# Kernel optimization log

Measured on AMD Instinct MI355X. Metric: run time of the kernel, lower is better.

The kernel has to match this reference:

```python
import jax, jax.numpy as jnp
import numpy as np

D = 1024
H = 16
DK = D // H  # 64
CHUNK = 64
EPS = 1e-5


def setup_inputs() -> dict:
    key = jax.random.key(0)
    k1, k2, k3 = jax.random.split(key, 3)
    x = jax.random.normal(k1, (4, 4096, D), dtype=jnp.float32)
    W_qkv = jax.random.normal(k2, (D, 3 * D), dtype=jnp.float32) * 0.02
    W_o = jax.random.normal(k3, (D, D), dtype=jnp.float32) * 0.02
    return {"x": x, "W_qkv": W_qkv, "W_o": W_o}


def _layernorm_noaffine(k):
    mu = jnp.mean(k, axis=-1, keepdims=True)
    var = jnp.mean((k - mu) ** 2, axis=-1, keepdims=True)  # biased var, torch LayerNorm
    return (k - mu) / jnp.sqrt(var + EPS)


def _linear_attn(x, W_qkv, W_o):
    B, L, Dm = x.shape
    qkv = (x @ W_qkv).reshape(B, L, 3, H, DK)
    q, k, v = qkv[:, :, 0], qkv[:, :, 1], qkv[:, :, 2]
    k = _layernorm_noaffine(k)

    nC = L // CHUNK
    # [nC, B, C, H, DK] for scan over chunks
    to_chunks = lambda t: t.reshape(B, nC, CHUNK, H, DK).transpose(1, 0, 2, 3, 4)
    qc, kc, vc = to_chunks(q), to_chunks(k), to_chunks(v)

    causal = jnp.tril(jnp.ones((CHUNK, CHUNK), dtype=bool))  # s <= t inclusive

    def step(S, chunk):
        q_c, k_c, v_c = chunk  # each [B, C, H, DK]
        # inter-chunk: y_t += S_prev @ q_t
        inter = jnp.einsum('bhde,bthe->bthd', S, q_c)
        # intra-chunk: y_t += sum_{s<=t} (k_s . q_t) v_s
        scores = jnp.einsum('bthd,bshd->bhts', q_c, k_c)
        scores = jnp.where(causal, scores, 0.0)
        intra = jnp.einsum('bhts,bshd->bthd', scores, v_c)
        # state update: S += sum_t v_t k_t^T
        S = S + jnp.einsum('bthd,bthe->bhde', v_c, k_c)
        return S, inter + intra

    S0 = jnp.zeros((B, H, DK, DK), dtype=x.dtype)
    _, ys = jax.lax.scan(step, S0, (qc, kc, vc))  # ys: [nC, B, C, H, DK]
    y = ys.transpose(1, 0, 2, 3, 4).reshape(B, L, Dm)
    return y @ W_o


def reference(x, W_qkv, W_o):
    return _linear_attn(x, W_qkv, W_o)
```

## Files before the change

kernel.cpp:

```cpp
#include <hip/hip_runtime.h>

#define EPS 1e-5f

typedef __attribute__((ext_vector_type(8))) short s16x8;
typedef __attribute__((ext_vector_type(4))) float f4;

__device__ __forceinline__ short f2bf(float f) {
  union { float f; unsigned u; } x; x.f = f;
  unsigned r = x.u + 0x7fffu + ((x.u >> 16) & 1u);
  return (short)(r >> 16);
}
__device__ __forceinline__ float bf2f(short s) {
  union { unsigned u; float f; } x; x.u = ((unsigned)(unsigned short)s) << 16;
  return x.f;
}
__device__ __forceinline__ void gll16(const short* g, short* l) {
  __builtin_amdgcn_global_load_lds((const __attribute__((address_space(1))) void*)g,
                                   (__attribute__((address_space(3))) void*)l, 16, 0, 0);
}

#define BAR() asm volatile("s_barrier" ::: "memory")
#define LGKM0() do { asm volatile("s_waitcnt lgkmcnt(0)" ::: "memory"); \
                     __builtin_amdgcn_sched_barrier(0); } while (0)

__global__ __launch_bounds__(256) void prep(
    const float* __restrict__ x, const float* __restrict__ Wqkv,
    const float* __restrict__ Wo,
    short* __restrict__ xb, short* __restrict__ WqkvT, short* __restrict__ WoT)
{
  __shared__ float tile[32][33];
  const int bid = blockIdx.x;
  if (bid < 8192) {
    const size_t i = ((size_t)bid * 256 + threadIdx.x) * 8;
    const float4* p = reinterpret_cast<const float4*>(x + i);
    float4 a = p[0], b = p[1];
    union { uint4 v; short s[8]; } o;
    o.s[0] = f2bf(a.x); o.s[1] = f2bf(a.y); o.s[2] = f2bf(a.z); o.s[3] = f2bf(a.w);
    o.s[4] = f2bf(b.x); o.s[5] = f2bf(b.y); o.s[6] = f2bf(b.z); o.s[7] = f2bf(b.w);
    *reinterpret_cast<uint4*>(xb + i) = o.v;
    return;
  }
  const float* W; short* WT; int K, N, t;
  if (bid < 11264) { W = Wqkv; WT = WqkvT; K = 1024; N = 3072; t = bid - 8192;  }
  else             { W = Wo;   WT = WoT;   K = 1024; N = 1024; t = bid - 11264; }
  const int nblk = N >> 5;
  const int n0 = (t % nblk) * 32, k0 = (t / nblk) * 32;
  const int tx = threadIdx.x & 31, ty = threadIdx.x >> 5;
  #pragma unroll
  for (int i = 0; i < 4; i++) {
    int r = ty + i * 8;
    tile[r][tx] = W[(size_t)(k0 + r) * N + n0 + tx];
  }
  __syncthreads();
  #pragma unroll
  for (int i = 0; i < 4; i++) {
    int r = ty + i * 8;
    WT[(size_t)(n0 + r) * K + k0 + tx] = f2bf(tile[tx][r]);
  }
}

__device__ __forceinline__ void stage_slice(const short* __restrict__ G, short* dstbase,
                                            int row0, int kcol, int rowgrp, int panel, int lane) {
  short* dst = dstbase + panel * 8192 + rowgrp * 512;
  const short* src = G + (size_t)(row0 + rowgrp * 16 + (lane >> 2)) * 1024
                       + kcol + panel * 32 + (((lane & 3) << 3) ^ ((lane >> 5) << 4));
  gll16(src, dst);
}

template<bool STAGE>
__device__ __forceinline__ void ktile8p(
    const short* ldsAc, const short* ldsBc, short* ldsAn, short* ldsBn,
    const short* __restrict__ A, const short* __restrict__ BT,
    int m0, int n0, int knext,
    int w, int lane, int wm, int wn, int quad, int l16,
    f4 (&acc)[8][4])
{
  s16x8 bfr[4][2];
  const int co = (quad << 3) ^ ((l16 >> 3) << 4);
  #pragma unroll
  for (int p = 0; p < 4; ++p) {
    s16x8 a00, a01, a10, a11;
    {
      const int r0 = (wm * 128 + p * 32 + l16) * 32;
      a00 = *reinterpret_cast<const s16x8*>(&ldsAc[r0 + co]);
      a01 = *reinterpret_cast<const s16x8*>(&ldsAc[8192 + r0 + co]);
      a10 = *reinterpret_cast<const s16x8*>(&ldsAc[r0 + 512 + co]);
      a11 = *reinterpret_cast<const s16x8*>(&ldsAc[8192 + r0 + 512 + co]);
    }
    if (p == 0) {
      #pragma unroll
      for (int nf = 0; nf < 4; ++nf) {
        const int rb = (wn * 64 + nf * 16 + l16) * 32;
        bfr[nf][0] = *reinterpret_cast<const s16x8*>(&ldsBc[rb + co]);
        bfr[nf][1] = *reinterpret_cast<const s16x8*>(&ldsBc[8192 + rb + co]);
      }
    }
    if (STAGE) {
      if (p == 0)      { stage_slice(BT, ldsBn, n0, knext, w,     0, lane); stage_slice(BT, ldsBn, n0, knext, w,     1, lane); }
      else if (p == 1) { stage_slice(BT, ldsBn, n0, knext, 8 + w, 0, lane); stage_slice(BT, ldsBn, n0, knext, 8 + w, 1, lane); }
      else if (p == 2) { const int rg = (w & 3) + ((w >> 2) << 3);
                         stage_slice(A, ldsAn, m0, knext, rg, 0, lane); stage_slice(A, ldsAn, m0, knext, rg, 1, lane); }
      else             { const int rg = 4 + (w & 3) + ((w >> 2) << 3);
                         stage_slice(A, ldsAn, m0, knext, rg, 0, lane); stage_slice(A, ldsAn, m0, knext, rg, 1, lane); }
    }
    BAR();
    LGKM0();
    __builtin_amdgcn_s_setprio(1);
    #pragma unroll
    for (int nf = 0; nf < 4; ++nf) {
      acc[2*p  ][nf] = __builtin_amdgcn_mfma_f32_16x16x32_bf16(a00, bfr[nf][0], acc[2*p  ][nf], 0, 0, 0);
      acc[2*p  ][nf] = __builtin_amdgcn_mfma_f32_16x16x32_bf16(a01, bfr[nf][1], acc[2*p  ][nf], 0, 0, 0);
      acc[2*p+1][nf] = __builtin_amdgcn_mfma_f32_16x16x32_bf16(a10, bfr[nf][0], acc[2*p+1][nf], 0, 0, 0);
      acc[2*p+1][nf] = __builtin_amdgcn_mfma_f32_16x16x32_bf16(a11, bfr[nf][1], acc[2*p+1][nf], 0, 0, 0);
    }
    __builtin_amdgcn_s_setprio(0);
    if (p == 1) {
      if (STAGE) asm volatile("s_waitcnt vmcnt(4)" ::: "memory");
      else       asm volatile("s_waitcnt vmcnt(0)" ::: "memory");
    }
    if (p == 3 && STAGE) asm volatile("s_waitcnt vmcnt(2)" ::: "memory");
    BAR();
  }
}

#define GEMM8P_PROLOGUE()                                                            \
  stage_slice(BT, Bb0, n0, 0, w,     0, lane); stage_slice(BT, Bb0, n0, 0, w,     1, lane); \
  stage_slice(BT, Bb0, n0, 0, 8 + w, 0, lane); stage_slice(BT, Bb0, n0, 0, 8 + w, 1, lane); \
  { const int rg = (w & 3) + ((w >> 2) << 3);                                        \
    stage_slice(A, Ab0, m0, 0, rg, 0, lane); stage_slice(A, Ab0, m0, 0, rg, 1, lane); } \
  { const int rg = 4 + (w & 3) + ((w >> 2) << 3);                                    \
    stage_slice(A, Ab0, m0, 0, rg, 0, lane); stage_slice(A, Ab0, m0, 0, rg, 1, lane); } \
  asm volatile("s_waitcnt vmcnt(2)" ::: "memory");                                   \
  BAR()

#define GEMM8P_MAINLOOP()                                                            \
  _Pragma("unroll 1")                                                                \
  for (int t = 0; t < 14; t += 2) {                                                  \
    ktile8p<true>(Ab0, Bb0, Ab1, Bb1, A, BT, m0, n0, (t + 1) << 6, w, lane, wm, wn, quad, l16, acc); \
    ktile8p<true>(Ab1, Bb1, Ab0, Bb0, A, BT, m0, n0, (t + 2) << 6, w, lane, wm, wn, quad, l16, acc); \
  }                                                                                  \
  ktile8p<true >(Ab0, Bb0, Ab1, Bb1, A, BT, m0, n0, 15 << 6, w, lane, wm, wn, quad, l16, acc); \
  ktile8p<false>(Ab1, Bb1, Ab0, Bb0, A, BT, m0, n0, 0,       w, lane, wm, wn, quad, l16, acc)

__global__ __launch_bounds__(512, 2) void gemm_qkv_8p(
    const short* __restrict__ A, const short* __restrict__ BT,
    short* __restrict__ qb, short* __restrict__ kb, short* __restrict__ vb)
{
  extern __shared__ __align__(16) short lds[];
  short* Ab0 = lds;           short* Ab1 = lds + 16384;
  short* Bb0 = lds + 32768;   short* Bb1 = lds + 49152;

  const int pid = blockIdx.x;
  const int wg = (pid & 7) * 96 + (pid >> 3);
  const int mb = wg / 12, nb = wg % 12;
  const int m0 = mb * 256, n0 = nb * 256;

  const int tid = threadIdx.x;
  const int w = tid >> 6, lane = tid & 63, quad = lane >> 4, l16 = lane & 15;
  const int wm = w >> 2, wn = w & 3;

  f4 acc[8][4];
  #pragma unroll
  for (int i = 0; i < 8; i++)
    #pragma unroll
    for (int j = 0; j < 4; j++) acc[i][j] = {0.f, 0.f, 0.f, 0.f};

  GEMM8P_PROLOGUE();
  GEMM8P_MAINLOOP();

  __syncthreads();
  short* st = lds + w * 1152;
  const int j0 = n0 + wn * 64;
  const int sq = j0 >> 10;
  const int hh = (j0 >> 6) & 15;
  short* dbuf = (sq == 0) ? qb : (sq == 1) ? kb : vb;
  const int r2 = lane >> 3, c8 = (lane & 7) << 3;
  #pragma unroll
  for (int mf = 0; mf < 8; ++mf) {
    #pragma unroll
    for (int nf = 0; nf < 4; ++nf)
      #pragma unroll
      for (int r = 0; r < 4; ++r)
        st[(quad * 4 + r) * 72 + nf * 16 + l16] = f2bf(acc[mf][nf][r]);
    #pragma unroll
    for (int h2 = 0; h2 < 2; ++h2) {
      int rr = h2 * 8 + r2;
      int i = m0 + wm * 128 + mf * 16 + rr;
      int bb = i >> 12, ll = i & 4095;
      uint4 val = *reinterpret_cast<const uint4*>(&st[rr * 72 + c8]);
      *reinterpret_cast<uint4*>(&dbuf[(((size_t)(bb * 16 + hh)) * 4096 + ll) * 64 + c8]) = val;
    }
  }
}

__global__ __launch_bounds__(512, 2) void gemm_out_8p(
    const short* __restrict__ A, const short* __restrict__ BT, float* __restrict__ C)
{
  extern __shared__ __align__(16) short lds[];
  short* Ab0 = lds;           short* Ab1 = lds + 16384;
  short* Bb0 = lds + 32768;   short* Bb1 = lds + 49152;

  const int pid = blockIdx.x;
  const int wg = (pid & 7) * 32 + (pid >> 3);
  const int mb = wg >> 2, nb = wg & 3;
  const int m0 = mb * 256, n0 = nb * 256;

  const int tid = threadIdx.x;
  const int w = tid >> 6, lane = tid & 63, quad = lane >> 4, l16 = lane & 15;
  const int wm = w >> 2, wn = w & 3;

  f4 acc[8][4];
  #pragma unroll
  for (int i = 0; i < 8; i++)
    #pragma unroll
    for (int j = 0; j < 4; j++) acc[i][j] = {0.f, 0.f, 0.f, 0.f};

  GEMM8P_PROLOGUE();
  GEMM8P_MAINLOOP();

  #pragma unroll
  for (int mf = 0; mf < 8; ++mf)
    #pragma unroll
    for (int nf = 0; nf < 4; ++nf)
      #pragma unroll
      for (int r = 0; r < 4; ++r) {
        int i = m0 + wm * 128 + mf * 16 + quad * 4 + r;
        int j = n0 + wn * 64 + nf * 16 + l16;
        C[(size_t)i * 1024 + j] = acc[mf][nf][r];
      }
}

__global__ __launch_bounds__(256) void gemm_qkv_v4(
    const short* __restrict__ A, const short* __restrict__ BT,
    short* __restrict__ qb, short* __restrict__ kb, short* __restrict__ vb)
{
  __shared__ __align__(16) short lds[8192];
  short* As = lds;
  short* Bs = lds + 4096;

  const int p = blockIdx.x;
  const int slot = p >> 3;
  const int strip = (p & 7) + 8 * (slot / 24);
  const int nb = slot % 24;
  const int m0 = strip * 128, n0 = nb * 128;

  const int tid = threadIdx.x;
  const int w = tid >> 6, lane = tid & 63, quad = lane >> 4, l16 = lane & 15;
  const int wm = (w >> 1) << 6, wn = (w & 1) << 6;

  f4 acc[4][4];
  #pragma unroll
  for (int i = 0; i < 4; i++)
    #pragma unroll
    for (int j = 0; j < 4; j++) acc[i][j] = {0.f, 0.f, 0.f, 0.f};

  const int row = w * 32 + (lane >> 2), ofs = (lane & 3) << 3;

  for (int k0 = 0; k0 < 1024; k0 += 32) {
    __syncthreads();
    gll16(A + (size_t)(m0 + row) * 1024 + k0 + ofs, &As[(w * 32) * 32]);
    gll16(A + (size_t)(m0 + row + 16) * 1024 + k0 + ofs, &As[(w * 32 + 16) * 32]);
    gll16(BT + (size_t)(n0 + row) * 1024 + k0 + ofs, &Bs[(w * 32) * 32]);
    gll16(BT + (size_t)(n0 + row + 16) * 1024 + k0 + ofs, &Bs[(w * 32 + 16) * 32]);
    __syncthreads();
    s16x8 afr[4], bfr[4];
    #pragma unroll
    for (int t = 0; t < 4; t++)
      afr[t] = *reinterpret_cast<const s16x8*>(&As[(wm + t * 16 + l16) * 32 + quad * 8]);
    #pragma unroll
    for (int t = 0; t < 4; t++)
      bfr[t] = *reinterpret_cast<const s16x8*>(&Bs[(wn + t * 16 + l16) * 32 + quad * 8]);
    #pragma unroll
    for (int ti = 0; ti < 4; ti++)
      #pragma unroll
      for (int tj = 0; tj < 4; tj++)
        acc[ti][tj] = __builtin_amdgcn_mfma_f32_16x16x32_bf16(afr[ti], bfr[tj], acc[ti][tj], 0, 0, 0);
  }

  __syncthreads();
  short* st = &lds[w * 16 * 72];
  const int j0 = n0 + wn;
  const int sq = j0 >> 10;
  const int hh = (j0 >> 6) & 15;
  short* dbuf = (sq == 0) ? qb : (sq == 1) ? kb : vb;
  const int r2 = lane >> 3, c8 = (lane & 7) << 3;
  #pragma unroll
  for (int ti = 0; ti < 4; ti++) {
    #pragma unroll
    for (int tj = 0; tj < 4; tj++)
      #pragma unroll
      for (int r = 0; r < 4; r++)
        st[(quad * 4 + r) * 72 + tj * 16 + l16] = f2bf(acc[ti][tj][r]);
    #pragma unroll
    for (int h2 = 0; h2 < 2; h2++) {
      int rr = h2 * 8 + r2;
      int i = m0 + wm + ti * 16 + rr;
      int bb = i >> 12, ll = i & 4095;
      uint4 val = *reinterpret_cast<const uint4*>(&st[rr * 72 + c8]);
      *reinterpret_cast<uint4*>(&dbuf[(((size_t)(bb * 16 + hh)) * 4096 + ll) * 64 + c8]) = val;
    }
  }
}

__global__ __launch_bounds__(256) void ln_k(short* __restrict__ kbuf)
{
  const int row = blockIdx.x * 4 + (threadIdx.x >> 6);
  const int lane = threadIdx.x & 63;
  const size_t idx = (size_t)row * 64 + lane;
  float v = bf2f(kbuf[idx]);
  float s = v, s2 = v * v;
  #pragma unroll
  for (int off = 32; off; off >>= 1) {
    s += __shfl_xor(s, off);
    s2 += __shfl_xor(s2, off);
  }
  float mean = s * (1.f / 64.f);
  float var = s2 * (1.f / 64.f) - mean * mean;
  float rstd = rsqrtf(var + EPS);
  kbuf[idx] = f2bf((v - mean) * rstd);
}

__global__ __launch_bounds__(256) void chunk_outer(
    const short* __restrict__ kb, const short* __restrict__ vb,
    short* __restrict__ G)
{
  __shared__ __align__(16) short kT[64 * 72];
  __shared__ __align__(16) short vT[64 * 72];
  const int bh = blockIdx.x >> 6, c = blockIdx.x & 63;
  const int tid = threadIdx.x;
  const int w = tid >> 6, lane = tid & 63, quad = lane >> 4, l16 = lane & 15;
  const int srow = tid >> 2, sseg = (tid & 3) << 4;
  const size_t base = (size_t)bh * 262144 + (size_t)(c * 64 + srow) * 64 + sseg;
  const int toff = ((((srow >> 3) ^ ((tid & 3) << 1)) & 7) << 3) + (srow & 7);

  {
    const float4* kp = reinterpret_cast<const float4*>(kb + base);
    union { float4 v[2]; short s[16]; } ku;
    ku.v[0] = kp[0]; ku.v[1] = kp[1];
    float kv[16]; float s = 0.f, s2 = 0.f;
    #pragma unroll
    for (int i = 0; i < 16; i++) { kv[i] = bf2f(ku.s[i]); s += kv[i]; s2 += kv[i] * kv[i]; }
    s += __shfl_xor(s, 1);  s2 += __shfl_xor(s2, 1);
    s += __shfl_xor(s, 2);  s2 += __shfl_xor(s2, 2);
    float mean = s * (1.f / 64.f);
    float var = s2 * (1.f / 64.f) - mean * mean;
    float rstd = rsqrtf(var + EPS);
    #pragma unroll
    for (int i = 0; i < 16; i++) kT[(sseg + i) * 72 + toff] = f2bf((kv[i] - mean) * rstd);
    const float4* vp = reinterpret_cast<const float4*>(vb + base);
    union { float4 v[2]; short s[16]; } vu;
    vu.v[0] = vp[0]; vu.v[1] = vp[1];
    #pragma unroll
    for (int i = 0; i < 16; i++) vT[(sseg + i) * 72 + toff] = vu.s[i];
  }
  __syncthreads();
  const int gsw = (w & 3) << 1;
  s16x8 va0 = *reinterpret_cast<const s16x8*>(&vT[(w * 16 + l16) * 72 + ((quad ^ gsw) << 3)]);
  s16x8 va1 = *reinterpret_cast<const s16x8*>(&vT[(w * 16 + l16) * 72 + (((4 + quad) ^ gsw) << 3)]);
  short* Gc = G + ((size_t)blockIdx.x) * 4096;
  #pragma unroll
  for (int tj = 0; tj < 4; tj++) {
    const int gk = (tj & 3) << 1;
    s16x8 kb0 = *reinterpret_cast<const s16x8*>(&kT[(tj * 16 + l16) * 72 + ((quad ^ gk) << 3)]);
    s16x8 kb1 = *reinterpret_cast<const s16x8*>(&kT[(tj * 16 + l16) * 72 + (((4 + quad) ^ gk) << 3)]);
    f4 z = {0.f, 0.f, 0.f, 0.f};
    z = __builtin_amdgcn_mfma_f32_16x16x32_bf16(va0, kb0, z, 0, 0, 0);
    z = __builtin_amdgcn_mfma_f32_16x16x32_bf16(va1, kb1, z, 0, 0, 0);
    #pragma unroll
    for (int r = 0; r < 4; r++)
      Gc[(w * 16 + quad * 4 + r) * 64 + tj * 16 + l16] = f2bf(z[r]);
  }
}

__global__ __launch_bounds__(128) void prefix_S(short* __restrict__ G)
{
  const int bh = blockIdx.x >> 3, rg = blockIdx.x & 7;
  short* p = G + (size_t)bh * 262144 + rg * 512 + threadIdx.x * 4;
  float s0 = 0.f, s1 = 0.f, s2 = 0.f, s3 = 0.f;
  union U { uint2 v; short s[4]; };
  U cur; cur.v = *reinterpret_cast<const uint2*>(p);
  #pragma unroll 4
  for (int c = 0; c < 64; c++) {
    short* pc = p + (size_t)c * 4096;
    U nxt;
    if (c < 63) nxt.v = *reinterpret_cast<const uint2*>(pc + 4096);
    float g0 = bf2f(cur.s[0]), g1 = bf2f(cur.s[1]), g2 = bf2f(cur.s[2]), g3 = bf2f(cur.s[3]);
    U su;
    su.s[0] = f2bf(s0); su.s[1] = f2bf(s1); su.s[2] = f2bf(s2); su.s[3] = f2bf(s3);
    *reinterpret_cast<uint2*>(pc) = su.v;
    s0 += g0; s1 += g1; s2 += g2; s3 += g3;
    cur = nxt;
  }
}

__global__ __launch_bounds__(256) void chunk_out(
    const short* __restrict__ qb, const short* __restrict__ kb,
    const short* __restrict__ vb, const short* __restrict__ S,
    short* __restrict__ yb)
{
  __shared__ __align__(16) short vT[64 * 72];
  __shared__ __align__(16) short Ps[64 * 72];
  const int bh = blockIdx.x >> 6, c = blockIdx.x & 63;
  const int b = bh >> 4, h = bh & 15;
  const int tid = threadIdx.x;
  const int w = tid >> 6, lane = tid & 63, quad = lane >> 4, l16 = lane & 15;
  const int srow = tid >> 2, sseg = (tid & 3) << 4;
  const size_t base = (size_t)bh * 262144 + (size_t)c * 4096;
  const int toff = ((((srow >> 3) ^ ((tid & 3) << 1)) & 7) << 3) + (srow & 7);

  {
    const float4* vp = reinterpret_cast<const float4*>(vb + base + (size_t)srow * 64 + sseg);
    union { float4 v[2]; short s[16]; } vu;
    vu.v[0] = vp[0]; vu.v[1] = vp[1];
    #pragma unroll
    for (int i = 0; i < 16; i++) vT[(sseg + i) * 72 + toff] = vu.s[i];
  }
  s16x8 qa[4][2], kf[2], sf[2];
  #pragma unroll
  for (int ti = 0; ti < 4; ti++)
    #pragma unroll
    for (int kh = 0; kh < 2; kh++)
      qa[ti][kh] = *reinterpret_cast<const s16x8*>(
          qb + base + (size_t)(ti * 16 + l16) * 64 + kh * 32 + quad * 8);
  #pragma unroll
  for (int kh = 0; kh < 2; kh++) {
    kf[kh] = *reinterpret_cast<const s16x8*>(
        kb + base + (size_t)(w * 16 + l16) * 64 + kh * 32 + quad * 8);
    sf[kh] = *reinterpret_cast<const s16x8*>(
        S + base + (size_t)(w * 16 + l16) * 64 + kh * 32 + quad * 8);
  }
  {
    float kv[16]; float s = 0.f, s2 = 0.f;
    #pragma unroll
    for (int kh = 0; kh < 2; kh++)
      #pragma unroll
      for (int i = 0; i < 8; i++) {
        float f = bf2f(kf[kh][i]); kv[kh * 8 + i] = f; s += f; s2 += f * f;
      }
    s += __shfl_xor(s, 16);  s2 += __shfl_xor(s2, 16);
    s += __shfl_xor(s, 32);  s2 += __shfl_xor(s2, 32);
    float mean = s * (1.f / 64.f);
    float var = s2 * (1.f / 64.f) - mean * mean;
    float rstd = rsqrtf(var + EPS);
    #pragma unroll
    for (int kh = 0; kh < 2; kh++)
      #pragma unroll
      for (int i = 0; i < 8; i++)
        kf[kh][i] = f2bf((kv[kh * 8 + i] - mean) * rstd);
  }
  __syncthreads();
  const int psoff = ((((w * 16 + l16) >> 3) ^ (quad << 1)) << 3) + (l16 & 7);
  #pragma unroll
  for (int ti = 0; ti < 4; ti++) {
    f4 z = {0.f, 0.f, 0.f, 0.f};
    z = __builtin_amdgcn_mfma_f32_16x16x32_bf16(qa[ti][0], kf[0], z, 0, 0, 0);
    z = __builtin_amdgcn_mfma_f32_16x16x32_bf16(qa[ti][1], kf[1], z, 0, 0, 0);
    #pragma unroll
    for (int r = 0; r < 4; r++) {
      int t = ti * 16 + quad * 4 + r;
      int s = w * 16 + l16;
      Ps[t * 72 + psoff] = (s <= t) ? f2bf(z[r]) : (short)0;
    }
  }
  __syncthreads();
  const int gsw = (w & 3) << 1;
  s16x8 vf0 = *reinterpret_cast<const s16x8*>(&vT[(w * 16 + l16) * 72 + ((quad ^ gsw) << 3)]);
  s16x8 vf1 = *reinterpret_cast<const s16x8*>(&vT[(w * 16 + l16) * 72 + (((4 + quad) ^ gsw) << 3)]);
  const int pf = ((l16 >> 2) & 3) << 1;
  #pragma unroll
  for (int ti = 0; ti < 4; ti++) {
    f4 z = {0.f, 0.f, 0.f, 0.f};
    s16x8 p0 = *reinterpret_cast<const s16x8*>(&Ps[(ti * 16 + l16) * 72 + ((quad ^ pf) << 3)]);
    s16x8 p1 = *reinterpret_cast<const s16x8*>(&Ps[(ti * 16 + l16) * 72 + (((4 + quad) ^ pf) << 3)]);
    z = __builtin_amdgcn_mfma_f32_16x16x32_bf16(p0, vf0, z, 0, 0, 0);
    z = __builtin_amdgcn_mfma_f32_16x16x32_bf16(p1, vf1, z, 0, 0, 0);
    z = __builtin_amdgcn_mfma_f32_16x16x32_bf16(qa[ti][0], sf[0], z, 0, 0, 0);
    z = __builtin_amdgcn_mfma_f32_16x16x32_bf16(qa[ti][1], sf[1], z, 0, 0, 0);
    #pragma unroll
    for (int r = 0; r < 4; r++) {
      int t = ti * 16 + quad * 4 + r;
      int d = w * 16 + l16;
      yb[(((size_t)b * 4096) + c * 64 + t) * 1024 + h * 64 + d] = f2bf(z[r]);
    }
  }
}

__global__ __launch_bounds__(256) void gemm_out_v3(
    const short* __restrict__ A, const short* __restrict__ BT, float* __restrict__ C)
{
  __shared__ __align__(16) short As[128 * 32];
  __shared__ __align__(16) short Bs[128 * 32];
  const int p = blockIdx.x;
  const int slot = p >> 3;
  const int strip = (p & 7) + 8 * (slot >> 3);
  const int nb = slot & 7;
  const int m0 = strip * 128, n0 = nb * 128;
  const int tid = threadIdx.x;
  const int w = tid >> 6, lane = tid & 63, quad = lane >> 4, l16 = lane & 15;
  const int wm = (w >> 1) << 6, wn = (w & 1) << 6;

  f4 acc[4][4];
  #pragma unroll
  for (int i = 0; i < 4; i++)
    #pragma unroll
    for (int j = 0; j < 4; j++) acc[i][j] = {0.f, 0.f, 0.f, 0.f};

  const int row = w * 32 + (lane >> 2), ofs = (lane & 3) << 3;

  for (int k0 = 0; k0 < 1024; k0 += 32) {
    __syncthreads();
    gll16(A + (size_t)(m0 + row) * 1024 + k0 + ofs, &As[(w * 32) * 32]);
    gll16(A + (size_t)(m0 + row + 16) * 1024 + k0 + ofs, &As[(w * 32 + 16) * 32]);
    gll16(BT + (size_t)(n0 + row) * 1024 + k0 + ofs, &Bs[(w * 32) * 32]);
    gll16(BT + (size_t)(n0 + row + 16) * 1024 + k0 + ofs, &Bs[(w * 32 + 16) * 32]);
    __syncthreads();
    s16x8 afr[4], bfr[4];
    #pragma unroll
    for (int t = 0; t < 4; t++)
      afr[t] = *reinterpret_cast<const s16x8*>(&As[(wm + t * 16 + l16) * 32 + quad * 8]);
    #pragma unroll
    for (int t = 0; t < 4; t++)
      bfr[t] = *reinterpret_cast<const s16x8*>(&Bs[(wn + t * 16 + l16) * 32 + quad * 8]);
    #pragma unroll
    for (int ti = 0; ti < 4; ti++)
      #pragma unroll
      for (int tj = 0; tj < 4; tj++)
        acc[ti][tj] = __builtin_amdgcn_mfma_f32_16x16x32_bf16(afr[ti], bfr[tj], acc[ti][tj], 0, 0, 0);
  }
  #pragma unroll
  for (int ti = 0; ti < 4; ti++)
    #pragma unroll
    for (int tj = 0; tj < 4; tj++)
      #pragma unroll
      for (int r = 0; r < 4; r++) {
        int i = m0 + wm + ti * 16 + quad * 4 + r;
        int j = n0 + wn + tj * 16 + l16;
        C[(size_t)i * 1024 + j] = acc[ti][tj][r];
      }
}

__global__ __launch_bounds__(256) void gemm_qkv_r1(
    const float* __restrict__ A, const float* __restrict__ B,
    short* __restrict__ qb, short* __restrict__ kb, short* __restrict__ vb)
{
  __shared__ __align__(16) short As[128 * 40];
  __shared__ __align__(16) short Bs[128 * 40];
  const int n0 = blockIdx.x * 128;
  const int m0 = blockIdx.y * 128;
  const int tid = threadIdx.x;
  const int w = tid >> 6, lane = tid & 63, quad = lane >> 4, l16 = lane & 15;
  const int wm = (w >> 1) << 6, wn = (w & 1) << 6;
  f4 acc[4][4];
  #pragma unroll
  for (int i = 0; i < 4; i++)
    #pragma unroll
    for (int j = 0; j < 4; j++) acc[i][j] = {0.f, 0.f, 0.f, 0.f};
  const int arow = tid >> 1, aseg = (tid & 1) << 4;
  const int brow = tid >> 3, bseg = (tid & 7) << 4;
  for (int k0 = 0; k0 < 1024; k0 += 32) {
    __syncthreads();
    {
      const float4* ap = reinterpret_cast<const float4*>(A + (size_t)(m0 + arow) * 1024 + k0 + aseg);
      union { float4 v[4]; float f[16]; } af;
      af.v[0] = ap[0]; af.v[1] = ap[1]; af.v[2] = ap[2]; af.v[3] = ap[3];
      union { float4 v[2]; short s[16]; } ao;
      #pragma unroll
      for (int i = 0; i < 16; i++) ao.s[i] = f2bf(af.f[i]);
      float4* dst = reinterpret_cast<float4*>(&As[arow * 40 + aseg]);
      dst[0] = ao.v[0]; dst[1] = ao.v[1];
    }
    {
      const float4* bp = reinterpret_cast<const float4*>(B + (size_t)(k0 + brow) * 3072 + n0 + bseg);
      union { float4 v[4]; float f[16]; } bu;
      bu.v[0] = bp[0]; bu.v[1] = bp[1]; bu.v[2] = bp[2]; bu.v[3] = bp[3];
      #pragma unroll
      for (int i = 0; i < 16; i++) Bs[(bseg + i) * 40 + brow] = f2bf(bu.f[i]);
    }
    __syncthreads();
    s16x8 afr[4], bfr[4];
    #pragma unroll
    for (int t = 0; t < 4; t++)
      afr[t] = *reinterpret_cast<const s16x8*>(&As[(wm + t * 16 + l16) * 40 + quad * 8]);
    #pragma unroll
    for (int t = 0; t < 4; t++)
      bfr[t] = *reinterpret_cast<const s16x8*>(&Bs[(wn + t * 16 + l16) * 40 + quad * 8]);
    #pragma unroll
    for (int ti = 0; ti < 4; ti++)
      #pragma unroll
      for (int tj = 0; tj < 4; tj++)
        acc[ti][tj] = __builtin_amdgcn_mfma_f32_16x16x32_bf16(afr[ti], bfr[tj], acc[ti][tj], 0, 0, 0);
  }
  const int sq = n0 >> 10;
  short* dbuf = (sq == 0) ? qb : (sq == 1) ? kb : vb;
  #pragma unroll
  for (int ti = 0; ti < 4; ti++)
    #pragma unroll
    for (int tj = 0; tj < 4; tj++)
      #pragma unroll
      for (int r = 0; r < 4; r++) {
        int i = m0 + wm + ti * 16 + quad * 4 + r;
        int j = n0 + wn + tj * 16 + l16;
        int hh = (j >> 6) & 15, dd = j & 63;
        int bb = i >> 12, ll = i & 4095;
        dbuf[(((size_t)(bb * 16 + hh)) * 4096 + ll) * 64 + dd] = f2bf(acc[ti][tj][r]);
      }
}

__global__ __launch_bounds__(256) void scan_chunks_r1(
    const short* __restrict__ qb, const short* __restrict__ kb,
    const short* __restrict__ vb, short* __restrict__ yb)
{
  __shared__ __align__(16) short qs[64 * 72];
  __shared__ __align__(16) short ks[64 * 72];
  __shared__ __align__(16) short kT[64 * 72];
  __shared__ __align__(16) short vT[64 * 72];
  __shared__ __align__(16) short Sb[64 * 72];
  __shared__ __align__(16) short Ps[64 * 72];
  const int bh = blockIdx.x;
  const int b = bh >> 4, h = bh & 15;
  const int tid = threadIdx.x;
  const int w = tid >> 6, lane = tid & 63, quad = lane >> 4, l16 = lane & 15;
  const int srow = tid >> 2, sseg = (tid & 3) << 4;
  const size_t base = (size_t)bh * 4096 * 64;
  f4 accS[4];
  #pragma unroll
  for (int i = 0; i < 4; i++) accS[i] = {0.f, 0.f, 0.f, 0.f};
  for (int c = 0; c < 64; c++) {
    __syncthreads();
    {
      size_t g = base + ((size_t)(c * 64 + srow)) * 64 + sseg;
      const float4* qp = reinterpret_cast<const float4*>(qb + g);
      float4 q0 = qp[0], q1 = qp[1];
      *reinterpret_cast<float4*>(&qs[srow * 72 + sseg]) = q0;
      *reinterpret_cast<float4*>(&qs[srow * 72 + sseg + 8]) = q1;
      const float4* kp = reinterpret_cast<const float4*>(kb + g);
      union { float4 v[2]; short s[16]; } ku;
      ku.v[0] = kp[0]; ku.v[1] = kp[1];
      *reinterpret_cast<float4*>(&ks[srow * 72 + sseg]) = ku.v[0];
      *reinterpret_cast<float4*>(&ks[srow * 72 + sseg + 8]) = ku.v[1];
      #pragma unroll
      for (int i = 0; i < 16; i++) kT[(sseg + i) * 72 + srow] = ku.s[i];
      const float4* vp = reinterpret_cast<const float4*>(vb + g);
      union { float4 v[2]; short s[16]; } vu;
      vu.v[0] = vp[0]; vu.v[1] = vp[1];
      #pragma unroll
      for (int i = 0; i < 16; i++) vT[(sseg + i) * 72 + srow] = vu.s[i];
    }
    #pragma unroll
    for (int ti = 0; ti < 4; ti++)
      #pragma unroll
      for (int r = 0; r < 4; r++)
        Sb[(ti * 16 + quad * 4 + r) * 72 + w * 16 + l16] = f2bf(accS[ti][r]);
    __syncthreads();
    s16x8 qa[4][2];
    #pragma unroll
    for (int ti = 0; ti < 4; ti++)
      #pragma unroll
      for (int kh = 0; kh < 2; kh++)
        qa[ti][kh] = *reinterpret_cast<const s16x8*>(&qs[(ti * 16 + l16) * 72 + kh * 32 + quad * 8]);
    s16x8 kf[2];
    #pragma unroll
    for (int kh = 0; kh < 2; kh++)
      kf[kh] = *reinterpret_cast<const s16x8*>(&ks[(w * 16 + l16) * 72 + kh * 32 + quad * 8]);
    #pragma unroll
    for (int ti = 0; ti < 4; ti++) {
      f4 z = {0.f, 0.f, 0.f, 0.f};
      z = __builtin_amdgcn_mfma_f32_16x16x32_bf16(qa[ti][0], kf[0], z, 0, 0, 0);
      z = __builtin_amdgcn_mfma_f32_16x16x32_bf16(qa[ti][1], kf[1], z, 0, 0, 0);
      #pragma unroll
      for (int r = 0; r < 4; r++) {
        int t = ti * 16 + quad * 4 + r;
        int s = w * 16 + l16;
        Ps[t * 72 + s] = (s <= t) ? f2bf(z[r]) : (short)0;
      }
    }
    __syncthreads();
    s16x8 vf[2], sf[2];
    #pragma unroll
    for (int kh = 0; kh < 2; kh++) {
      vf[kh] = *reinterpret_cast<const s16x8*>(&vT[(w * 16 + l16) * 72 + kh * 32 + quad * 8]);
      sf[kh] = *reinterpret_cast<const s16x8*>(&Sb[(w * 16 + l16) * 72 + kh * 32 + quad * 8]);
    }
    #pragma unroll
    for (int ti = 0; ti < 4; ti++) {
      f4 z = {0.f, 0.f, 0.f, 0.f};
      s16x8 p0 = *reinterpret_cast<const s16x8*>(&Ps[(ti * 16 + l16) * 72 + quad * 8]);
      s16x8 p1 = *reinterpret_cast<const s16x8*>(&Ps[(ti * 16 + l16) * 72 + 32 + quad * 8]);
      z = __builtin_amdgcn_mfma_f32_16x16x32_bf16(p0, vf[0], z, 0, 0, 0);
      z = __builtin_amdgcn_mfma_f32_16x16x32_bf16(p1, vf[1], z, 0, 0, 0);
      z = __builtin_amdgcn_mfma_f32_16x16x32_bf16(qa[ti][0], sf[0], z, 0, 0, 0);
      z = __builtin_amdgcn_mfma_f32_16x16x32_bf16(qa[ti][1], sf[1], z, 0, 0, 0);
      #pragma unroll
      for (int r = 0; r < 4; r++) {
        int t = ti * 16 + quad * 4 + r;
        int d = w * 16 + l16;
        yb[(((size_t)b * 4096) + c * 64 + t) * 1024 + h * 64 + d] = f2bf(z[r]);
      }
    }
    s16x8 ku0 = *reinterpret_cast<const s16x8*>(&kT[(w * 16 + l16) * 72 + quad * 8]);
    s16x8 ku1 = *reinterpret_cast<const s16x8*>(&kT[(w * 16 + l16) * 72 + 32 + quad * 8]);
    #pragma unroll
    for (int ti = 0; ti < 4; ti++) {
      s16x8 va0 = *reinterpret_cast<const s16x8*>(&vT[(ti * 16 + l16) * 72 + quad * 8]);
      s16x8 va1 = *reinterpret_cast<const s16x8*>(&vT[(ti * 16 + l16) * 72 + 32 + quad * 8]);
      accS[ti] = __builtin_amdgcn_mfma_f32_16x16x32_bf16(va0, ku0, accS[ti], 0, 0, 0);
      accS[ti] = __builtin_amdgcn_mfma_f32_16x16x32_bf16(va1, ku1, accS[ti], 0, 0, 0);
    }
  }
}

__global__ __launch_bounds__(256) void gemm_out_r1(
    const short* __restrict__ A, const float* __restrict__ B, float* __restrict__ C)
{
  __shared__ __align__(16) short As[128 * 40];
  __shared__ __align__(16) short Bs[128 * 40];
  const int n0 = blockIdx.x * 128;
  const int m0 = blockIdx.y * 128;
  const int tid = threadIdx.x;
  const int w = tid >> 6, lane = tid & 63, quad = lane >> 4, l16 = lane & 15;
  const int wm = (w >> 1) << 6, wn = (w & 1) << 6;
  f4 acc[4][4];
  #pragma unroll
  for (int i = 0; i < 4; i++)
    #pragma unroll
    for (int j = 0; j < 4; j++) acc[i][j] = {0.f, 0.f, 0.f, 0.f};
  const int arow = tid >> 1, aseg = (tid & 1) << 4;
  const int brow = tid >> 3, bseg = (tid & 7) << 4;
  for (int k0 = 0; k0 < 1024; k0 += 32) {
    __syncthreads();
    {
      const float4* ap = reinterpret_cast<const float4*>(A + (size_t)(m0 + arow) * 1024 + k0 + aseg);
      float4 a0 = ap[0], a1 = ap[1];
      float4* dst = reinterpret_cast<float4*>(&As[arow * 40 + aseg]);
      dst[0] = a0; dst[1] = a1;
    }
    {
      const float4* bp = reinterpret_cast<const float4*>(B + (size_t)(k0 + brow) * 1024 + n0 + bseg);
      union { float4 v[4]; float f[16]; } bu;
      bu.v[0] = bp[0]; bu.v[1] = bp[1]; bu.v[2] = bp[2]; bu.v[3] = bp[3];
      #pragma unroll
      for (int i = 0; i < 16; i++) Bs[(bseg + i) * 40 + brow] = f2bf(bu.f[i]);
    }
    __syncthreads();
    s16x8 afr[4], bfr[4];
    #pragma unroll
    for (int t = 0; t < 4; t++)
      afr[t] = *reinterpret_cast<const s16x8*>(&As[(wm + t * 16 + l16) * 40 + quad * 8]);
    #pragma unroll
    for (int t = 0; t < 4; t++)
      bfr[t] = *reinterpret_cast<const s16x8*>(&Bs[(wn + t * 16 + l16) * 40 + quad * 8]);
    #pragma unroll
    for (int ti = 0; ti < 4; ti++)
      #pragma unroll
      for (int tj = 0; tj < 4; tj++)
        acc[ti][tj] = __builtin_amdgcn_mfma_f32_16x16x32_bf16(afr[ti], bfr[tj], acc[ti][tj], 0, 0, 0);
  }
  #pragma unroll
  for (int ti = 0; ti < 4; ti++)
    #pragma unroll
    for (int tj = 0; tj < 4; tj++)
      #pragma unroll
      for (int r = 0; r < 4; r++) {
        int i = m0 + wm + ti * 16 + quad * 4 + r;
        int j = n0 + wn + tj * 16 + l16;
        C[(size_t)i * 1024 + j] = acc[ti][tj][r];
      }
}

extern "C" void kernel_launch(void* const* d_in, const int* in_sizes, int n_in,
                              void* d_out, int out_size, void* d_ws, size_t ws_size,
                              hipStream_t stream) {
  const float* x    = (const float*)d_in[0];
  const float* Wqkv = (const float*)d_in[1];
  const float* Wo   = (const float*)d_in[2];
  float* out = (float*)d_out;

  short* qb = (short*)d_ws;
  short* kb = qb + (size_t)16777216;
  short* vb = kb + (size_t)16777216;
  short* yb = vb + (size_t)16777216;

  const size_t NEED = 176160768;
  if (ws_size >= NEED) {
    short* Gs    = yb + (size_t)16777216;
    short* WqkvT = Gs + (size_t)16777216;
    short* WoT   = WqkvT + (size_t)3145728;
    short* xb    = Gs;

    static int use8p = -1;
    if (use8p < 0) {
      hipError_t e1 = hipFuncSetAttribute((const void*)gemm_qkv_8p,
          hipFuncAttributeMaxDynamicSharedMemorySize, 131072);
      hipError_t e2 = hipFuncSetAttribute((const void*)gemm_out_8p,
          hipFuncAttributeMaxDynamicSharedMemorySize, 131072);
      use8p = (e1 == hipSuccess && e2 == hipSuccess) ? 1 : 0;
    }

    prep          <<<dim3(12288),   256, 0, stream>>>(x, Wqkv, Wo, xb, WqkvT, WoT);
    if (use8p)
      gemm_qkv_8p <<<dim3(768),     512, 131072, stream>>>(xb, WqkvT, qb, kb, vb);
    else
      gemm_qkv_v4 <<<dim3(3072),    256, 0, stream>>>(xb, WqkvT, qb, kb, vb);
    chunk_outer   <<<dim3(4096),    256, 0, stream>>>(kb, vb, Gs);
    prefix_S      <<<dim3(512),     128, 0, stream>>>(Gs);
    chunk_out     <<<dim3(4096),    256, 0, stream>>>(qb, kb, vb, Gs, yb);
    if (use8p)
      gemm_out_8p <<<dim3(256),     512, 131072, stream>>>(yb, WoT, out);
    else
      gemm_out_v3 <<<dim3(1024),    256, 0, stream>>>(yb, WoT, out);
  } else {
    gemm_qkv_r1   <<<dim3(24, 128), 256, 0, stream>>>(x, Wqkv, qb, kb, vb);
    ln_k          <<<dim3(65536),   256, 0, stream>>>(kb);
    scan_chunks_r1<<<dim3(64),      256, 0, stream>>>(qb, kb, vb, yb);
    gemm_out_r1   <<<dim3(8, 128),  256, 0, stream>>>(yb, Wo, out);
  }
}
```

Measured before the change: 321.1 us.

## Group chunks into macro-chunks of four with in-block state recurrence

Changes the chunked linear-attention scan from per-64-token chunks to 256-token macro-chunks. The outer-product kernel accumulates four chunks' v·k^T per block, the prefix scan runs over 16 macro-states instead of 64, and the output kernel walks its four chunks sequentially, updating the running state in registers with MFMA after each chunk. This cuts state traffic to global memory and the length of the prefix pass by a factor of four. In exchange, each output block has a serial four-step dependency and grids shrink from 4096 to 1024 blocks, which lowers parallelism. It also uses more LDS per block.

```diff
diff --git a/kernel.cpp b/kernel.cpp
--- a/kernel.cpp
+++ b/kernel.cpp
@@ -320,70 +320,78 @@
   kbuf[idx] = f2bf((v - mean) * rstd);
 }
 
-__global__ __launch_bounds__(256) void chunk_outer(
+__global__ __launch_bounds__(256) void macro_outer(
     const short* __restrict__ kb, const short* __restrict__ vb,
     short* __restrict__ G)
 {
   __shared__ __align__(16) short kT[64 * 72];
   __shared__ __align__(16) short vT[64 * 72];
-  const int bh = blockIdx.x >> 6, c = blockIdx.x & 63;
+  const int bh = blockIdx.x >> 4, mc = blockIdx.x & 15;
   const int tid = threadIdx.x;
   const int w = tid >> 6, lane = tid & 63, quad = lane >> 4, l16 = lane & 15;
   const int srow = tid >> 2, sseg = (tid & 3) << 4;
-  const size_t base = (size_t)bh * 262144 + (size_t)(c * 64 + srow) * 64 + sseg;
   const int toff = ((((srow >> 3) ^ ((tid & 3) << 1)) & 7) << 3) + (srow & 7);
-
-  {
-    const float4* kp = reinterpret_cast<const float4*>(kb + base);
-    union { float4 v[2]; short s[16]; } ku;
-    ku.v[0] = kp[0]; ku.v[1] = kp[1];
-    float kv[16]; float s = 0.f, s2 = 0.f;
-    #pragma unroll
-    for (int i = 0; i < 16; i++) { kv[i] = bf2f(ku.s[i]); s += kv[i]; s2 += kv[i] * kv[i]; }
-    s += __shfl_xor(s, 1);  s2 += __shfl_xor(s2, 1);
-    s += __shfl_xor(s, 2);  s2 += __shfl_xor(s2, 2);
-    float mean = s * (1.f / 64.f);
-    float var = s2 * (1.f / 64.f) - mean * mean;
-    float rstd = rsqrtf(var + EPS);
-    #pragma unroll
-    for (int i = 0; i < 16; i++) kT[(sseg + i) * 72 + toff] = f2bf((kv[i] - mean) * rstd);
-    const float4* vp = reinterpret_cast<const float4*>(vb + base);
-    union { float4 v[2]; short s[16]; } vu;
-    vu.v[0] = vp[0]; vu.v[1] = vp[1];
-    #pragma unroll
-    for (int i = 0; i < 16; i++) vT[(sseg + i) * 72 + toff] = vu.s[i];
-  }
-  __syncthreads();
   const int gsw = (w & 3) << 1;
-  s16x8 va0 = *reinterpret_cast<const s16x8*>(&vT[(w * 16 + l16) * 72 + ((quad ^ gsw) << 3)]);
-  s16x8 va1 = *reinterpret_cast<const s16x8*>(&vT[(w * 16 + l16) * 72 + (((4 + quad) ^ gsw) << 3)]);
-  short* Gc = G + ((size_t)blockIdx.x) * 4096;
-  #pragma unroll
-  for (int tj = 0; tj < 4; tj++) {
-    const int gk = (tj & 3) << 1;
-    s16x8 kb0 = *reinterpret_cast<const s16x8*>(&kT[(tj * 16 + l16) * 72 + ((quad ^ gk) << 3)]);
-    s16x8 kb1 = *reinterpret_cast<const s16x8*>(&kT[(tj * 16 + l16) * 72 + (((4 + quad) ^ gk) << 3)]);
-    f4 z = {0.f, 0.f, 0.f, 0.f};
-    z = __builtin_amdgcn_mfma_f32_16x16x32_bf16(va0, kb0, z, 0, 0, 0);
-    z = __builtin_amdgcn_mfma_f32_16x16x32_bf16(va1, kb1, z, 0, 0, 0);
+
+  f4 accG[4];
+  #pragma unroll
+  for (int tj = 0; tj < 4; tj++) accG[tj] = {0.f, 0.f, 0.f, 0.f};
+
+  for (int j = 0; j < 4; ++j) {
+    if (j) __syncthreads();
+    const size_t base = (size_t)bh * 262144 + (size_t)((mc * 4 + j) * 64 + srow) * 64 + sseg;
+    {
+      const float4* kp = reinterpret_cast<const float4*>(kb + base);
+      union { float4 v[2]; short s[16]; } ku;
+      ku.v[0] = kp[0]; ku.v[1] = kp[1];
+      float kv[16]; float s = 0.f, s2 = 0.f;
+      #pragma unroll
+      for (int i = 0; i < 16; i++) { kv[i] = bf2f(ku.s[i]); s += kv[i]; s2 += kv[i] * kv[i]; }
+      s += __shfl_xor(s, 1);  s2 += __shfl_xor(s2, 1);
+      s += __shfl_xor(s, 2);  s2 += __shfl_xor(s2, 2);
+      float mean = s * (1.f / 64.f);
+      float var = s2 * (1.f / 64.f) - mean * mean;
+      float rstd = rsqrtf(var + EPS);
+      #pragma unroll
+      for (int i = 0; i < 16; i++) kT[(sseg + i) * 72 + toff] = f2bf((kv[i] - mean) * rstd);
+      const float4* vp = reinterpret_cast<const float4*>(vb + base);
+      union { float4 v[2]; short s[16]; } vu;
+      vu.v[0] = vp[0]; vu.v[1] = vp[1];
+      #pragma unroll
+      for (int i = 0; i < 16; i++) vT[(sseg + i) * 72 + toff] = vu.s[i];
+    }
+    __syncthreads();
+    s16x8 va0 = *reinterpret_cast<const s16x8*>(&vT[(w * 16 + l16) * 72 + ((quad ^ gsw) << 3)]);
+    s16x8 va1 = *reinterpret_cast<const s16x8*>(&vT[(w * 16 + l16) * 72 + (((4 + quad) ^ gsw) << 3)]);
+    #pragma unroll
+    for (int tj = 0; tj < 4; tj++) {
+      const int gk = tj << 1;
+      s16x8 kb0 = *reinterpret_cast<const s16x8*>(&kT[(tj * 16 + l16) * 72 + ((quad ^ gk) << 3)]);
+      s16x8 kb1 = *reinterpret_cast<const s16x8*>(&kT[(tj * 16 + l16) * 72 + (((4 + quad) ^ gk) << 3)]);
+      accG[tj] = __builtin_amdgcn_mfma_f32_16x16x32_bf16(va0, kb0, accG[tj], 0, 0, 0);
+      accG[tj] = __builtin_amdgcn_mfma_f32_16x16x32_bf16(va1, kb1, accG[tj], 0, 0, 0);
+    }
+  }
+  short* Gc = G + (size_t)blockIdx.x * 4096;
+  #pragma unroll
+  for (int tj = 0; tj < 4; tj++)
     #pragma unroll
     for (int r = 0; r < 4; r++)
-      Gc[(w * 16 + quad * 4 + r) * 64 + tj * 16 + l16] = f2bf(z[r]);
-  }
-}
-
-__global__ __launch_bounds__(128) void prefix_S(short* __restrict__ G)
+      Gc[(w * 16 + quad * 4 + r) * 64 + tj * 16 + l16] = f2bf(accG[tj][r]);
+}
+
+__global__ __launch_bounds__(128) void prefix_S16(short* __restrict__ G)
 {
   const int bh = blockIdx.x >> 3, rg = blockIdx.x & 7;
-  short* p = G + (size_t)bh * 262144 + rg * 512 + threadIdx.x * 4;
+  short* p = G + (size_t)bh * 65536 + rg * 512 + threadIdx.x * 4;
   float s0 = 0.f, s1 = 0.f, s2 = 0.f, s3 = 0.f;
   union U { uint2 v; short s[4]; };
   U cur; cur.v = *reinterpret_cast<const uint2*>(p);
   #pragma unroll 4
-  for (int c = 0; c < 64; c++) {
-    short* pc = p + (size_t)c * 4096;
-    U nxt;
-    if (c < 63) nxt.v = *reinterpret_cast<const uint2*>(pc + 4096);
+  for (int mc = 0; mc < 16; mc++) {
+    short* pc = p + (size_t)mc * 4096;
+    U nxt; nxt.v = cur.v;
+    if (mc < 15) nxt.v = *reinterpret_cast<const uint2*>(pc + 4096);
     float g0 = bf2f(cur.s[0]), g1 = bf2f(cur.s[1]), g2 = bf2f(cur.s[2]), g3 = bf2f(cur.s[3]);
     U su;
     su.s[0] = f2bf(s0); su.s[1] = f2bf(s1); su.s[2] = f2bf(s2); su.s[3] = f2bf(s3);
@@ -393,94 +401,124 @@
   }
 }
 
-__global__ __launch_bounds__(256) void chunk_out(
+__global__ __launch_bounds__(256) void macro_out(
     const short* __restrict__ qb, const short* __restrict__ kb,
-    const short* __restrict__ vb, const short* __restrict__ S,
+    const short* __restrict__ vb, const short* __restrict__ G,
     short* __restrict__ yb)
 {
+  __shared__ __align__(16) short ks[64 * 72];
+  __shared__ __align__(16) short kT[64 * 72];
   __shared__ __align__(16) short vT[64 * 72];
+  __shared__ __align__(16) short Sb[64 * 72];
   __shared__ __align__(16) short Ps[64 * 72];
-  const int bh = blockIdx.x >> 6, c = blockIdx.x & 63;
+  const int bh = blockIdx.x >> 4, mc = blockIdx.x & 15;
   const int b = bh >> 4, h = bh & 15;
   const int tid = threadIdx.x;
   const int w = tid >> 6, lane = tid & 63, quad = lane >> 4, l16 = lane & 15;
   const int srow = tid >> 2, sseg = (tid & 3) << 4;
-  const size_t base = (size_t)bh * 262144 + (size_t)c * 4096;
   const int toff = ((((srow >> 3) ^ ((tid & 3) << 1)) & 7) << 3) + (srow & 7);
-
-  {
-    const float4* vp = reinterpret_cast<const float4*>(vb + base + (size_t)srow * 64 + sseg);
-    union { float4 v[2]; short s[16]; } vu;
-    vu.v[0] = vp[0]; vu.v[1] = vp[1];
-    #pragma unroll
-    for (int i = 0; i < 16; i++) vT[(sseg + i) * 72 + toff] = vu.s[i];
-  }
-  s16x8 qa[4][2], kf[2], sf[2];
-  #pragma unroll
-  for (int ti = 0; ti < 4; ti++)
-    #pragma unroll
-    for (int kh = 0; kh < 2; kh++)
-      qa[ti][kh] = *reinterpret_cast<const s16x8*>(
-          qb + base + (size_t)(ti * 16 + l16) * 64 + kh * 32 + quad * 8);
-  #pragma unroll
-  for (int kh = 0; kh < 2; kh++) {
-    kf[kh] = *reinterpret_cast<const s16x8*>(
-        kb + base + (size_t)(w * 16 + l16) * 64 + kh * 32 + quad * 8);
-    sf[kh] = *reinterpret_cast<const s16x8*>(
-        S + base + (size_t)(w * 16 + l16) * 64 + kh * 32 + quad * 8);
-  }
-  {
-    float kv[16]; float s = 0.f, s2 = 0.f;
-    #pragma unroll
-    for (int kh = 0; kh < 2; kh++)
-      #pragma unroll
-      for (int i = 0; i < 8; i++) {
-        float f = bf2f(kf[kh][i]); kv[kh * 8 + i] = f; s += f; s2 += f * f;
+  const int gsw = (w & 3) << 1;
+  const int rq2 = ((l16 >> 2) & 3) << 1;
+
+  const short* Sg = G + (size_t)blockIdx.x * 4096;
+  f4 accS[4];
+  #pragma unroll
+  for (int tj = 0; tj < 4; tj++)
+    #pragma unroll
+    for (int r = 0; r < 4; r++)
+      accS[tj][r] = bf2f(Sg[(w * 16 + quad * 4 + r) * 64 + tj * 16 + l16]);
+
+  for (int j = 0; j < 4; ++j) {
+    const int c = mc * 4 + j;
+    if (j) __syncthreads();
+    #pragma unroll
+    for (int tj = 0; tj < 4; tj++) {
+      const int eb = (tj << 1) + (l16 >> 3);
+      const int sbc = (((eb ^ (quad << 1)) & 7) << 3) + (l16 & 7);
+      #pragma unroll
+      for (int r = 0; r < 4; r++)
+        Sb[(w * 16 + quad * 4 + r) * 72 + sbc] = f2bf(accS[tj][r]);
+    }
+    const size_t base = (size_t)bh * 262144 + (size_t)(c * 64 + srow) * 64 + sseg;
+    {
+      const float4* kp = reinterpret_cast<const float4*>(kb + base);
+      union { float4 v[2]; short s[16]; } ku;
+      ku.v[0] = kp[0]; ku.v[1] = kp[1];
+      float kv[16]; float s = 0.f, s2 = 0.f;
+      #pragma unroll
+      for (int i = 0; i < 16; i++) { kv[i] = bf2f(ku.s[i]); s += kv[i]; s2 += kv[i] * kv[i]; }
+      s += __shfl_xor(s, 1);  s2 += __shfl_xor(s2, 1);
+      s += __shfl_xor(s, 2);  s2 += __shfl_xor(s2, 2);
+      float mean = s * (1.f / 64.f);
+      float var = s2 * (1.f / 64.f) - mean * mean;
+      float rstd = rsqrtf(var + EPS);
+      union { float4 v[2]; short s[16]; } ko;
+      #pragma unroll
+      for (int i = 0; i < 16; i++) ko.s[i] = f2bf((kv[i] - mean) * rstd);
+      *reinterpret_cast<float4*>(&ks[srow * 72 + sseg]) = ko.v[0];
+      *reinterpret_cast<float4*>(&ks[srow * 72 + sseg + 8]) = ko.v[1];
+      #pragma unroll
+      for (int i = 0; i < 16; i++) kT[(sseg + i) * 72 + toff] = ko.s[i];
+      const float4* vp = reinterpret_cast<const float4*>(vb + base);
+      union { float4 v[2]; short s[16]; } vu;
+      vu.v[0] = vp[0]; vu.v[1] = vp[1];
+      #pragma unroll
+      for (int i = 0; i < 16; i++) vT[(sseg + i) * 72 + toff] = vu.s[i];
+    }
+    s16x8 qa[4][2];
+    const size_t qbase = (size_t)bh * 262144 + (size_t)c * 4096;
+    #pragma unroll
+    for (int ti = 0; ti < 4; ti++)
+      #pragma unroll
+      for (int kh = 0; kh < 2; kh++)
+        qa[ti][kh] = *reinterpret_cast<const s16x8*>(
+            qb + qbase + (size_t)(ti * 16 + l16) * 64 + kh * 32 + quad * 8);
+    __syncthreads();
+    s16x8 kf[2], sf[2];
+    #pragma unroll
+    for (int kh = 0; kh < 2; kh++) {
+      kf[kh] = *reinterpret_cast<const s16x8*>(&ks[(w * 16 + l16) * 72 + kh * 32 + quad * 8]);
+      sf[kh] = *reinterpret_cast<const s16x8*>(&Sb[(w * 16 + l16) * 72 + ((((kh << 2) + quad) ^ rq2) << 3)]);
+    }
+    const int psoff = (((((w * 16 + l16) >> 3) ^ (quad << 1)) & 7) << 3) + (l16 & 7);
+    #pragma unroll
+    for (int ti = 0; ti < 4; ti++) {
+      f4 z = {0.f, 0.f, 0.f, 0.f};
+      z = __builtin_amdgcn_mfma_f32_16x16x32_bf16(qa[ti][0], kf[0], z, 0, 0, 0);
+      z = __builtin_amdgcn_mfma_f32_16x16x32_bf16(qa[ti][1], kf[1], z, 0, 0, 0);
+      #pragma unroll
+      for (int r = 0; r < 4; r++) {
+        int t = ti * 16 + quad * 4 + r;
+        int s = w * 16 + l16;
+        Ps[t * 72 + psoff] = (s <= t) ? f2bf(z[r]) : (short)0;
       }
-    s += __shfl_xor(s, 16);  s2 += __shfl_xor(s2, 16);
-    s += __shfl_xor(s, 32);  s2 += __shfl_xor(s2, 32);
-    float mean = s * (1.f / 64.f);
-    float var = s2 * (1.f / 64.f) - mean * mean;
-    float rstd = rsqrtf(var + EPS);
-    #pragma unroll
-    for (int kh = 0; kh < 2; kh++)
-      #pragma unroll
-      for (int i = 0; i < 8; i++)
-        kf[kh][i] = f2bf((kv[kh * 8 + i] - mean) * rstd);
-  }
-  __syncthreads();
-  const int psoff = ((((w * 16 + l16) >> 3) ^ (quad << 1)) << 3) + (l16 & 7);
-  #pragma unroll
-  for (int ti = 0; ti < 4; ti++) {
-    f4 z = {0.f, 0.f, 0.f, 0.f};
-    z = __builtin_amdgcn_mfma_f32_16x16x32_bf16(qa[ti][0], kf[0], z, 0, 0, 0);
-    z = __builtin_amdgcn_mfma_f32_16x16x32_bf16(qa[ti][1], kf[1], z, 0, 0, 0);
-    #pragma unroll
-    for (int r = 0; r < 4; r++) {
-      int t = ti * 16 + quad * 4 + r;
-      int s = w * 16 + l16;
-      Ps[t * 72 + psoff] = (s <= t) ? f2bf(z[r]) : (short)0;
-    }
-  }
-  __syncthreads();
-  const int gsw = (w & 3) << 1;
-  s16x8 vf0 = *reinterpret_cast<const s16x8*>(&vT[(w * 16 + l16) * 72 + ((quad ^ gsw) << 3)]);
-  s16x8 vf1 = *reinterpret_cast<const s16x8*>(&vT[(w * 16 + l16) * 72 + (((4 + quad) ^ gsw) << 3)]);
-  const int pf = ((l16 >> 2) & 3) << 1;
-  #pragma unroll
-  for (int ti = 0; ti < 4; ti++) {
-    f4 z = {0.f, 0.f, 0.f, 0.f};
-    s16x8 p0 = *reinterpret_cast<const s16x8*>(&Ps[(ti * 16 + l16) * 72 + ((quad ^ pf) << 3)]);
-    s16x8 p1 = *reinterpret_cast<const s16x8*>(&Ps[(ti * 16 + l16) * 72 + (((4 + quad) ^ pf) << 3)]);
-    z = __builtin_amdgcn_mfma_f32_16x16x32_bf16(p0, vf0, z, 0, 0, 0);
-    z = __builtin_amdgcn_mfma_f32_16x16x32_bf16(p1, vf1, z, 0, 0, 0);
-    z = __builtin_amdgcn_mfma_f32_16x16x32_bf16(qa[ti][0], sf[0], z, 0, 0, 0);
-    z = __builtin_amdgcn_mfma_f32_16x16x32_bf16(qa[ti][1], sf[1], z, 0, 0, 0);
-    #pragma unroll
-    for (int r = 0; r < 4; r++) {
-      int t = ti * 16 + quad * 4 + r;
-      int d = w * 16 + l16;
-      yb[(((size_t)b * 4096) + c * 64 + t) * 1024 + h * 64 + d] = f2bf(z[r]);
+    }
+    __syncthreads();
+    s16x8 vf0 = *reinterpret_cast<const s16x8*>(&vT[(w * 16 + l16) * 72 + ((quad ^ gsw) << 3)]);
+    s16x8 vf1 = *reinterpret_cast<const s16x8*>(&vT[(w * 16 + l16) * 72 + (((4 + quad) ^ gsw) << 3)]);
+    #pragma unroll
+    for (int ti = 0; ti < 4; ti++) {
+      f4 z = {0.f, 0.f, 0.f, 0.f};
+      s16x8 p0 = *reinterpret_cast<const s16x8*>(&Ps[(ti * 16 + l16) * 72 + ((quad ^ rq2) << 3)]);
+      s16x8 p1 = *reinterpret_cast<const s16x8*>(&Ps[(ti * 16 + l16) * 72 + (((4 + quad) ^ rq2) << 3)]);
+      z = __builtin_amdgcn_mfma_f32_16x16x32_bf16(p0, vf0, z, 0, 0, 0);
+      z = __builtin_amdgcn_mfma_f32_16x16x32_bf16(p1, vf1, z, 0, 0, 0);
+      z = __builtin_amdgcn_mfma_f32_16x16x32_bf16(qa[ti][0], sf[0], z, 0, 0, 0);
+      z = __builtin_amdgcn_mfma_f32_16x16x32_bf16(qa[ti][1], sf[1], z, 0, 0, 0);
+      #pragma unroll
+      for (int r = 0; r < 4; r++) {
+        int t = ti * 16 + quad * 4 + r;
+        int d = w * 16 + l16;
+        yb[(((size_t)b * 4096) + c * 64 + t) * 1024 + h * 64 + d] = f2bf(z[r]);
+      }
+    }
+    #pragma unroll
+    for (int tj = 0; tj < 4; tj++) {
+      const int gk = tj << 1;
+      s16x8 ub0 = *reinterpret_cast<const s16x8*>(&kT[(tj * 16 + l16) * 72 + ((quad ^ gk) << 3)]);
+      s16x8 ub1 = *reinterpret_cast<const s16x8*>(&kT[(tj * 16 + l16) * 72 + (((4 + quad) ^ gk) << 3)]);
+      accS[tj] = __builtin_amdgcn_mfma_f32_16x16x32_bf16(vf0, ub0, accS[tj], 0, 0, 0);
+      accS[tj] = __builtin_amdgcn_mfma_f32_16x16x32_bf16(vf1, ub1, accS[tj], 0, 0, 0);
     }
   }
 }
@@ -801,9 +839,9 @@
       gemm_qkv_8p <<<dim3(768),     512, 131072, stream>>>(xb, WqkvT, qb, kb, vb);
     else
       gemm_qkv_v4 <<<dim3(3072),    256, 0, stream>>>(xb, WqkvT, qb, kb, vb);
-    chunk_outer   <<<dim3(4096),    256, 0, stream>>>(kb, vb, Gs);
-    prefix_S      <<<dim3(512),     128, 0, stream>>>(Gs);
-    chunk_out     <<<dim3(4096),    256, 0, stream>>>(qb, kb, vb, Gs, yb);
+    macro_outer   <<<dim3(1024),    256, 0, stream>>>(kb, vb, Gs);
+    prefix_S16    <<<dim3(512),     128, 0, stream>>>(Gs);
+    macro_out     <<<dim3(1024),    256, 0, stream>>>(qb, kb, vb, Gs, yb);
     if (use8p)
       gemm_out_8p <<<dim3(256),     512, 131072, stream>>>(yb, WoT, out);
     else
```

After: 302.9 us, median of 2. -5.7%, faster.
